# Kernel optimization log

Measured on AMD Instinct MI355X. Metric: run time of the kernel, lower is better.

## Reference

```python
import jax, jax.numpy as jnp
import numpy as np

LN_EPS = 1e-12  # default nn.LayerNorm eps used by the HF ViT config


def setup_inputs() -> dict:
    key = jax.random.key(0)
    ks = jax.random.split(key, 6)
    B, H, S, D = 2, 12, 197, 768
    Hd = D // H
    hidden_states = jax.random.normal(ks[0], (B, S, D), jnp.float32)
    # attention probs: softmax-normalized over last axis for realism
    logits = jax.random.normal(ks[1], (B, H, S, S), jnp.float32)
    attention_probs = jax.nn.softmax(logits, axis=-1)
    value_layer = jax.random.normal(ks[2], (B, H, S, Hd), jnp.float32)
    dense_weight = jax.random.normal(ks[3], (D, D), jnp.float32) * 0.02
    ln_weight = jax.random.uniform(ks[4], (D,), jnp.float32, 0.5, 1.5)
    pre_ln_states = jax.random.normal(ks[5], (B, S, D), jnp.float32)
    return {
        'hidden_states': hidden_states,
        'attention_probs': attention_probs,
        'value_layer': value_layer,
        'dense_weight': dense_weight,
        'ln_weight': ln_weight,
        'pre_ln_states': pre_ln_states,
    }


def _norm(x):
    return jnp.linalg.norm(x, axis=-1)


def _diag_bsd(x):
    # torch.diagonal(x, dim1=1, dim2=2).permute(0,2,1): (b,k,s,d)->(b,s,d)
    return jnp.transpose(jnp.diagonal(x, axis1=1, axis2=2), (0, 2, 1))


def reference(hidden_states, attention_probs, value_layer, dense_weight, ln_weight, pre_ln_states):
    B, S, D = hidden_states.shape
    H = attention_probs.shape[1]
    Hd = D // H
    # dense.weight.view(all_head, H, Hd)
    dw = dense_weight.reshape(D, H, Hd)
    transformed = jnp.einsum('bhsv,dhv->bhsd', value_layer, dw)          # (B,H,S,D)
    weighted = jnp.einsum('bhks,bhsd->bhksd', attention_probs, transformed)  # (B,H,S,S,D)
    weighted_norm = _norm(weighted)                                       # (B,H,S,S)
    summed = weighted.sum(axis=1)                                         # (B,S,S,D)
    summed_norm = _norm(summed)
    residual = jnp.einsum('sk,bsd->bskd', jnp.eye(S, dtype=hidden_states.dtype), hidden_states)
    residual_weighted = summed + residual                                 # (B,S,S,D)
    residual_weighted_norm = _norm(residual_weighted)
    # LayerNorm decomposition: variance from pre_ln_states, mean per-component
    mean = pre_ln_states.mean(-1, keepdims=True)                          # (B,S,1)
    var = ((pre_ln_states - mean) ** 2).mean(-1, keepdims=True)[:, :, None]  # (B,S,1,1)
    each_mean = residual_weighted.mean(-1, keepdims=True)
    normalized = (residual_weighted - each_mean) / jnp.sqrt(var + LN_EPS)
    post_ln = normalized * ln_weight                                      # (B,S,S,D)
    post_ln_norm = _norm(post_ln)
    # mixing ratios
    def mixing_ratio(x):
        preserving = _diag_bsd(x)
        mixing = x.sum(axis=2) - preserving
        pn, mn = _norm(preserving), _norm(mixing)
        return mn / (mn + pn)
    attn_mix = mixing_ratio(summed)
    attnres_mix = mixing_ratio(residual_weighted)
    attnresln_mix = mixing_ratio(post_ln)
    return (weighted_norm, summed_norm, residual_weighted_norm, post_ln_norm,
            post_ln, attn_mix, attnres_mix, attnresln_mix)
```

## Files before the change

kernel.cpp:

```cpp
#include <hip/hip_runtime.h>
#include <cstdint>

#define S_ 197
#define D_ 768
#define H_ 12
#define B_ 2
#define SS_ (S_*S_)

#define O_WN   0
#define O_SN   931416
#define O_RWN  1009034
#define O_PLNN 1086652
#define O_PLN  1164270
#define O_AM   60774894
#define O_ARM  60775288
#define O_ARLM 60775682

#define WS_WT   0
#define WS_T2   589824
#define WS_TN   4220928
#define WS_ACC  4225656
#define WS_SMU  4830840
#define WS_DIAG 4831628
#define WS_MUI  5134220

#define I_T 4
#define NIT 50
#define NC 2
#define JC 99

__device__ __forceinline__ float wred64(float v) {
#pragma unroll
  for (int off = 32; off > 0; off >>= 1) v += __shfl_xor(v, off);
  return v;
}

__device__ __forceinline__ void load12(const float* __restrict__ p, float t[12]) {
  const float4* q = (const float4*)p;
  float4 a = q[0], b = q[1], c = q[2];
  t[0]=a.x; t[1]=a.y; t[2]=a.z; t[3]=a.w;
  t[4]=b.x; t[5]=b.y; t[6]=b.z; t[7]=b.w;
  t[8]=c.x; t[9]=c.y; t[10]=c.z; t[11]=c.w;
}

__global__ __launch_bounds__(256) void kTranspose(const float* __restrict__ in,
                                                  float* __restrict__ outp) {
  __shared__ float tile[32][33];
  int x = blockIdx.x*32 + threadIdx.x;
  int y = blockIdx.y*32 + threadIdx.y;
#pragma unroll
  for (int k = 0; k < 32; k += 8) tile[threadIdx.y+k][threadIdx.x] = in[(y+k)*D_ + x];
  __syncthreads();
  x = blockIdx.y*32 + threadIdx.x;
  y = blockIdx.x*32 + threadIdx.y;
#pragma unroll
  for (int k = 0; k < 32; k += 8) outp[(y+k)*D_ + x] = tile[threadIdx.x][threadIdx.y+k];
}

#define TST 8
__global__ __launch_bounds__(256) void kTransform(const float* __restrict__ V,
                                                  const float* __restrict__ Wt,
                                                  float* __restrict__ T2,
                                                  float* __restrict__ tnorm) {
  int blk = blockIdx.x;
  int xcd = blk & 7; int slot = blk >> 3;
  int bh = xcd*3 + (slot % 3);
  int st = slot / 3;
  int h = bh % H_; int b = bh / H_;
  int s0 = st*TST; int ns = min(TST, S_ - s0);
  __shared__ float vt[TST*64];
  __shared__ float red[4][TST];
  int t = threadIdx.x;
  const float* Vbase = V + ((size_t)bh*S_ + s0)*64;
  for (int e = t; e < ns*64; e += 256) vt[e] = Vbase[e];
  __syncthreads();
  float acc2[TST];
#pragma unroll
  for (int s = 0; s < TST; s++) acc2[s] = 0.f;
  for (int g = 0; g < 3; g++) {
    int d = t + g*256;
    float acc[TST];
#pragma unroll
    for (int s = 0; s < TST; s++) acc[s] = 0.f;
    const float* wp = Wt + (size_t)h*64*D_ + d;
#pragma unroll 8
    for (int v = 0; v < 64; v++) {
      float wv = wp[(size_t)v*D_];
#pragma unroll
      for (int s = 0; s < TST; s++) acc[s] = fmaf(vt[s*64+v], wv, acc[s]);
    }
    for (int s = 0; s < ns; s++) {
      T2[((size_t)(b*S_ + s0+s)*H_ + h)*D_ + d] = acc[s];
      acc2[s] = fmaf(acc[s], acc[s], acc2[s]);
    }
  }
  int lane = t & 63, wq = t >> 6;
#pragma unroll
  for (int s = 0; s < TST; s++) {
    float v = wred64(acc2[s]);
    if (lane == 0) red[wq][s] = v;
  }
  __syncthreads();
  if (t < ns) {
    float v = red[0][t] + red[1][t] + red[2][t] + red[3][t];
    tnorm[bh*S_ + s0 + t] = sqrtf(v);
  }
}

__global__ __launch_bounds__(256) void kWeightedNorm(const float* __restrict__ attn,
                                                     const float* __restrict__ tnorm,
                                                     float* __restrict__ outp) {
  int idx = blockIdx.x*256 + threadIdx.x;
  if (idx < B_*H_*SS_) {
    int bh = idx / SS_;
    int s = idx % S_;
    outp[O_WN + idx] = fabsf(attn[idx]) * tnorm[bh*S_ + s];
  }
}

__global__ __launch_bounds__(768) void kMain(const float* __restrict__ attn,
                                             const float* __restrict__ hs,
                                             const float* __restrict__ lnw,
                                             const float* __restrict__ preln,
                                             const float* __restrict__ T2,
                                             float* __restrict__ outp,
                                             float* __restrict__ wsAccS,
                                             float* __restrict__ wsSmu,
                                             float* __restrict__ wsDiagS,
                                             float* __restrict__ wsMui) {
  int blk = blockIdx.x;
  int xcd = blk & 7; int slot = blk >> 3;
  int b = (xcd >> 2) & 1;
  int c = (xcd >> 1) & 1;
  int it = slot*2 + (xcd & 1);
  int i0 = it * I_T;
  int jc0 = c * JC;
  int jcE = min(jc0 + JC, S_);
  int jcW = jcE - jc0;
  int ni = min(I_T, S_ - i0);
  int tid = threadIdx.x;
  int lane = tid & 63, wv = tid >> 6;
  int dbase = lane * 12;

  __shared__ float ash[H_*I_T*JC];
  __shared__ float sAcc[I_T*D_];
  __shared__ float sSmu[12*I_T];

  int tot = H_*I_T*jcW;
  for (int e = tid; e < tot; e += 768) {
    int hh = e / (I_T*jcW); int rem = e - hh*(I_T*jcW);
    int ii = rem / jcW; int jj = rem - ii*jcW;
    int iG = i0 + ii;
    float v = 0.f;
    if (iG < S_) v = attn[((size_t)(b*H_ + hh)*S_ + iG)*S_ + (jc0 + jj)];
    ash[(hh*I_T + ii)*JC + jj] = v;
  }

  float w_[12];
  load12(lnw + dbase, w_);
  float w2s_l = 0.f;
#pragma unroll
  for (int m = 0; m < 12; m++) w2s_l = fmaf(w_[m], w_[m], w2s_l);
  float w2sum = wred64(w2s_l);

  float istd[I_T];
#pragma unroll
  for (int ii = 0; ii < I_T; ii++) {
    int iG = i0 + ii;
    istd[ii] = 0.f;
    if (iG < S_) {
      float x[12];
      load12(preln + (size_t)(b*S_ + iG)*D_ + dbase, x);
      float sx = 0.f, sx2 = 0.f;
#pragma unroll
      for (int m = 0; m < 12; m++) { sx += x[m]; sx2 = fmaf(x[m], x[m], sx2); }
      sx = wred64(sx); sx2 = wred64(sx2);
      float mu = sx * (1.0f/768.0f);
      float var = sx2 * (1.0f/768.0f) - mu*mu;
      istd[ii] = 1.0f / sqrtf(var + 1e-12f);
    }
  }

  float accS[I_T][12];
#pragma unroll
  for (int ii = 0; ii < I_T; ii++)
#pragma unroll
    for (int m = 0; m < 12; m++) accS[ii][m] = 0.f;
  float smu[I_T] = {0.f, 0.f, 0.f, 0.f};

  __syncthreads();

  for (int j = jc0 + wv; j < jcE; j += 12) {
    int jj = j - jc0;
    const float* tb = T2 + (size_t)(b*S_ + j)*H_*D_ + dbase;
    float s[I_T][12];
#pragma unroll
    for (int ii = 0; ii < I_T; ii++)
#pragma unroll
      for (int m = 0; m < 12; m++) s[ii][m] = 0.f;
#pragma unroll 2
    for (int h = 0; h < H_; h++) {
      float t[12];
      load12(tb + h*D_, t);
#pragma unroll
      for (int ii = 0; ii < I_T; ii++) {
        float ah = ash[(h*I_T + ii)*JC + jj];
#pragma unroll
        for (int m = 0; m < 12; m++) s[ii][m] = fmaf(ah, t[m], s[ii][m]);
      }
    }
#pragma unroll
    for (int ii = 0; ii < I_T; ii++) {
      int iG = i0 + ii;
      if (iG < S_) {
        bool isDiag = (j == iG);
        float rw[12];
        if (isDiag) {
          float hh[12];
          load12(hs + (size_t)(b*S_ + iG)*D_ + dbase, hh);
#pragma unroll
          for (int m = 0; m < 12; m++) rw[m] = s[ii][m] + hh[m];
        } else {
#pragma unroll
          for (int m = 0; m < 12; m++) rw[m] = s[ii][m];
        }
        float ls2 = 0.f, lrw = 0.f, lrw2 = 0.f, lrww2 = 0.f, lrw2w2 = 0.f;
#pragma unroll
        for (int m = 0; m < 12; m++) {
          ls2 = fmaf(s[ii][m], s[ii][m], ls2);
          lrw += rw[m];
          float t1 = rw[m] * w_[m];
          lrww2 = fmaf(t1, w_[m], lrww2);
          lrw2 = fmaf(rw[m], rw[m], lrw2);
          lrw2w2 = fmaf(t1, t1, lrw2w2);
        }
        ls2 = wred64(ls2); lrw = wred64(lrw); lrw2 = wred64(lrw2);
        lrww2 = wred64(lrww2); lrw2w2 = wred64(lrw2w2);
        float mu = lrw * (1.0f/768.0f);
        float q = fmaf(mu*mu, w2sum, fmaf(-2.0f*mu, lrww2, lrw2w2));
        float plnn = istd[ii] * sqrtf(fmaxf(q, 0.f));
        int oIdx = (b*S_ + iG)*S_ + j;
        if (lane == 0) {
          outp[O_SN + oIdx] = sqrtf(ls2);
          outp[O_RWN + oIdx] = sqrtf(lrw2);
          outp[O_PLNN + oIdx] = plnn;
        }
        float* po = outp + O_PLN + (size_t)oIdx*D_ + dbase;
        float a = istd[ii];
        float p[12];
#pragma unroll
        for (int m = 0; m < 12; m++) p[m] = (rw[m] - mu) * a * w_[m];
        *(float2*)po        = make_float2(p[0], p[1]);
        *(float4*)(po + 2)  = make_float4(p[2], p[3], p[4], p[5]);
        *(float4*)(po + 6)  = make_float4(p[6], p[7], p[8], p[9]);
        *(float2*)(po + 10) = make_float2(p[10], p[11]);
#pragma unroll
        for (int m = 0; m < 12; m++) accS[ii][m] += s[ii][m];
        smu[ii] += mu;
        if (isDiag) {
          float4* dp = (float4*)(wsDiagS + (size_t)(b*S_ + iG)*D_ + dbase);
          dp[0] = make_float4(s[ii][0], s[ii][1], s[ii][2],  s[ii][3]);
          dp[1] = make_float4(s[ii][4], s[ii][5], s[ii][6],  s[ii][7]);
          dp[2] = make_float4(s[ii][8], s[ii][9], s[ii][10], s[ii][11]);
          if (lane == 0) wsMui[b*S_ + iG] = mu;
        }
      }
    }
  }

  if (lane == 0) {
#pragma unroll
    for (int ii = 0; ii < I_T; ii++) sSmu[wv*I_T + ii] = smu[ii];
  }
  for (int rr = 0; rr < 12; rr++) {
    __syncthreads();
    if (wv == rr) {
#pragma unroll
      for (int ii = 0; ii < I_T; ii++) {
        if (ii < ni) {
#pragma unroll
          for (int m = 0; m < 12; m++) {
            int a = ii*D_ + dbase + m;
            sAcc[a] = (rr == 0) ? accS[ii][m] : (sAcc[a] + accS[ii][m]);
          }
        }
      }
    }
  }
  __syncthreads();
  if (tid < ni*192) {
    int ii = tid / 192; int d4 = (tid % 192) * 4;
    float4 v = *(float4*)&sAcc[ii*D_ + d4];
    *(float4*)(wsAccS + (size_t)((b*S_ + i0 + ii)*NC + c)*D_ + d4) = v;
  }
  if (tid < ni) {
    float ss = 0.f;
#pragma unroll
    for (int wq = 0; wq < 12; wq++) ss += sSmu[wq*I_T + tid];
    wsSmu[(b*S_ + i0 + tid)*NC + c] = ss;
  }
}

__global__ __launch_bounds__(256) void kMixing(const float* __restrict__ wsAccS,
                                               const float* __restrict__ wsSmu,
                                               const float* __restrict__ wsDiagS,
                                               const float* __restrict__ wsMui,
                                               const float* __restrict__ hs,
                                               const float* __restrict__ lnw,
                                               float* __restrict__ outp) {
  int bi = blockIdx.x;
  int t = threadIdx.x;
  float Smu = wsSmu[bi*2] + wsSmu[bi*2 + 1];
  float mui = wsMui[bi];
  float dmu = Smu - mui;
  float mS = 0.f, pS = 0.f, pRW = 0.f, mP = 0.f, pP = 0.f;
#pragma unroll
  for (int g = 0; g < 3; g++) {
    int d = t + g*256;
    float acc = wsAccS[(size_t)(bi*2)*D_ + d] + wsAccS[(size_t)(bi*2 + 1)*D_ + d];
    float dg = wsDiagS[(size_t)bi*D_ + d];
    float h = hs[(size_t)bi*D_ + d];
    float w = lnw[d];
    float mix = acc - dg;
    mS = fmaf(mix, mix, mS);
    pS = fmaf(dg, dg, pS);
    float drw = dg + h;
    pRW = fmaf(drw, drw, pRW);
    float mp = w * (mix - dmu);
    mP = fmaf(mp, mp, mP);
    float dp = w * (drw - mui);
    pP = fmaf(dp, dp, pP);
  }
  __shared__ float red[4][5];
  int lane = t & 63, wv = t >> 6;
  mS = wred64(mS); pS = wred64(pS); pRW = wred64(pRW); mP = wred64(mP); pP = wred64(pP);
  if (lane == 0) { red[wv][0]=mS; red[wv][1]=pS; red[wv][2]=pRW; red[wv][3]=mP; red[wv][4]=pP; }
  __syncthreads();
  if (t == 0) {
    float a0=0,a1=0,a2=0,a3=0,a4=0;
#pragma unroll
    for (int k = 0; k < 4; k++) { a0+=red[k][0]; a1+=red[k][1]; a2+=red[k][2]; a3+=red[k][3]; a4+=red[k][4]; }
    float mn = sqrtf(a0), pn = sqrtf(a1);
    outp[O_AM + bi] = mn / (mn + pn);
    float pnrw = sqrtf(a2);
    outp[O_ARM + bi] = mn / (mn + pnrw);
    float mnp = sqrtf(a3), pnp = sqrtf(a4);
    outp[O_ARLM + bi] = mnp / (mnp + pnp);
  }
}

extern "C" void kernel_launch(void* const* d_in, const int* in_sizes, int n_in,
                              void* d_out, int out_size, void* d_ws, size_t ws_size,
                              hipStream_t stream) {
  const float* hs    = (const float*)d_in[0];
  const float* attn  = (const float*)d_in[1];
  const float* V     = (const float*)d_in[2];
  const float* W     = (const float*)d_in[3];
  const float* lnw   = (const float*)d_in[4];
  const float* preln = (const float*)d_in[5];
  float* out = (float*)d_out;
  float* ws  = (float*)d_ws;

  kTranspose<<<dim3(24,24), dim3(32,8), 0, stream>>>(W, ws + WS_WT);
  kTransform<<<dim3(600), dim3(256), 0, stream>>>(V, ws + WS_WT, ws + WS_T2, ws + WS_TN);
  kWeightedNorm<<<dim3((B_*H_*SS_ + 255)/256), dim3(256), 0, stream>>>(attn, ws + WS_TN, out);
  kMain<<<dim3(B_*NIT*NC), dim3(768), 0, stream>>>(attn, hs, lnw, preln, ws + WS_T2, out,
                                                   ws + WS_ACC, ws + WS_SMU, ws + WS_DIAG, ws + WS_MUI);
  kMixing<<<dim3(B_*S_), dim3(256), 0, stream>>>(ws + WS_ACC, ws + WS_SMU, ws + WS_DIAG, ws + WS_MUI,
                                                 hs, lnw, out);
}
```

Baseline: 351.1 us.

## Fuse weighted-norm into main kernel, split columns four ways, reuse diagonal reductions

Removes the separate weighted-norm kernel by having the main kernel write |attn|*tnorm from its shared-memory attention tile, with per-head transform norms staged in shared memory. The column dimension is now split into four chunks across 400 blocks of 512 threads, replacing two chunks across 200 blocks of 768 threads. The diagonal term is left out of the accumulated sums, and its already-reduced norms are stored as three scalars, so the mixing kernel no longer reads the diagonal vectors or hidden states. The main trade-off is more partial-sum traffic in the mixing kernel, which now reads four accumulator rows per position instead of two.

```diff
diff --git a/kernel.cpp b/kernel.cpp
--- a/kernel.cpp
+++ b/kernel.cpp
@@ -16,18 +16,17 @@
 #define O_ARM  60775288
 #define O_ARLM 60775682
 
-#define WS_WT   0
-#define WS_T2   589824
-#define WS_TN   4220928
-#define WS_ACC  4225656
-#define WS_SMU  4830840
-#define WS_DIAG 4831628
-#define WS_MUI  5134220
+#define WS_T2   0
+#define WS_TN   3631104
+#define WS_ACC  3635832
+#define WS_WT   3635832
+#define WS_SMU  4846200
+#define WS_MUI  4847776
+#define WS_P3   4848170
 
 #define I_T 4
-#define NIT 50
-#define NC 2
-#define JC 99
+#define NC 4
+#define JCM 50
 
 __device__ __forceinline__ float wred64(float v) {
 #pragma unroll
@@ -107,53 +106,46 @@
   }
 }
 
-__global__ __launch_bounds__(256) void kWeightedNorm(const float* __restrict__ attn,
-                                                     const float* __restrict__ tnorm,
-                                                     float* __restrict__ outp) {
-  int idx = blockIdx.x*256 + threadIdx.x;
-  if (idx < B_*H_*SS_) {
-    int bh = idx / SS_;
-    int s = idx % S_;
-    outp[O_WN + idx] = fabsf(attn[idx]) * tnorm[bh*S_ + s];
-  }
-}
-
-__global__ __launch_bounds__(768) void kMain(const float* __restrict__ attn,
+__global__ __launch_bounds__(512) void kMain(const float* __restrict__ attn,
                                              const float* __restrict__ hs,
                                              const float* __restrict__ lnw,
                                              const float* __restrict__ preln,
                                              const float* __restrict__ T2,
+                                             const float* __restrict__ tnorm,
                                              float* __restrict__ outp,
                                              float* __restrict__ wsAccS,
                                              float* __restrict__ wsSmu,
-                                             float* __restrict__ wsDiagS,
-                                             float* __restrict__ wsMui) {
+                                             float* __restrict__ wsMui,
+                                             float* __restrict__ wsP) {
   int blk = blockIdx.x;
-  int xcd = blk & 7; int slot = blk >> 3;
-  int b = (xcd >> 2) & 1;
-  int c = (xcd >> 1) & 1;
-  int it = slot*2 + (xcd & 1);
+  int xcd = blk & 7; int it = blk >> 3;
+  int b = xcd >> 2;  int c = xcd & 3;
   int i0 = it * I_T;
-  int jc0 = c * JC;
-  int jcE = min(jc0 + JC, S_);
+  int jc0 = (c == 3) ? 149 : c*50;
+  int jcE = (c == 0) ? 50 : (c == 1) ? 100 : (c == 2) ? 149 : 197;
   int jcW = jcE - jc0;
   int ni = min(I_T, S_ - i0);
   int tid = threadIdx.x;
   int lane = tid & 63, wv = tid >> 6;
   int dbase = lane * 12;
 
-  __shared__ float ash[H_*I_T*JC];
+  __shared__ float ash[H_*I_T*JCM];
+  __shared__ float tnl[H_*JCM];
   __shared__ float sAcc[I_T*D_];
-  __shared__ float sSmu[12*I_T];
+  __shared__ float sSmu[8*I_T];
 
   int tot = H_*I_T*jcW;
-  for (int e = tid; e < tot; e += 768) {
+  for (int e = tid; e < tot; e += 512) {
     int hh = e / (I_T*jcW); int rem = e - hh*(I_T*jcW);
     int ii = rem / jcW; int jj = rem - ii*jcW;
     int iG = i0 + ii;
     float v = 0.f;
     if (iG < S_) v = attn[((size_t)(b*H_ + hh)*S_ + iG)*S_ + (jc0 + jj)];
-    ash[(hh*I_T + ii)*JC + jj] = v;
+    ash[(hh*I_T + ii)*JCM + jj] = v;
+  }
+  for (int e = tid; e < H_*jcW; e += 512) {
+    int hh = e / jcW; int jj = e - hh*jcW;
+    tnl[hh*JCM + jj] = tnorm[(b*H_ + hh)*S_ + jc0 + jj];
   }
 
   float w_[12];
@@ -190,7 +182,7 @@
 
   __syncthreads();
 
-  for (int j = jc0 + wv; j < jcE; j += 12) {
+  for (int j = jc0 + wv; j < jcE; j += 8) {
     int jj = j - jc0;
     const float* tb = T2 + (size_t)(b*S_ + j)*H_*D_ + dbase;
     float s[I_T][12];
@@ -204,7 +196,7 @@
       load12(tb + h*D_, t);
 #pragma unroll
       for (int ii = 0; ii < I_T; ii++) {
-        float ah = ash[(h*I_T + ii)*JC + jj];
+        float ah = ash[(h*I_T + ii)*JCM + jj];
 #pragma unroll
         for (int m = 0; m < 12; m++) s[ii][m] = fmaf(ah, t[m], s[ii][m]);
       }
@@ -238,7 +230,8 @@
         lrww2 = wred64(lrww2); lrw2w2 = wred64(lrw2w2);
         float mu = lrw * (1.0f/768.0f);
         float q = fmaf(mu*mu, w2sum, fmaf(-2.0f*mu, lrww2, lrw2w2));
-        float plnn = istd[ii] * sqrtf(fmaxf(q, 0.f));
+        q = fmaxf(q, 0.f);
+        float plnn = istd[ii] * sqrtf(q);
         int oIdx = (b*S_ + iG)*S_ + j;
         if (lane == 0) {
           outp[O_SN + oIdx] = sqrtf(ls2);
@@ -254,15 +247,17 @@
         *(float4*)(po + 2)  = make_float4(p[2], p[3], p[4], p[5]);
         *(float4*)(po + 6)  = make_float4(p[6], p[7], p[8], p[9]);
         *(float2*)(po + 10) = make_float2(p[10], p[11]);
-#pragma unroll
-        for (int m = 0; m < 12; m++) accS[ii][m] += s[ii][m];
         smu[ii] += mu;
         if (isDiag) {
-          float4* dp = (float4*)(wsDiagS + (size_t)(b*S_ + iG)*D_ + dbase);
-          dp[0] = make_float4(s[ii][0], s[ii][1], s[ii][2],  s[ii][3]);
-          dp[1] = make_float4(s[ii][4], s[ii][5], s[ii][6],  s[ii][7]);
-          dp[2] = make_float4(s[ii][8], s[ii][9], s[ii][10], s[ii][11]);
-          if (lane == 0) wsMui[b*S_ + iG] = mu;
+          if (lane == 0) {
+            wsMui[b*S_ + iG] = mu;
+            wsP[(b*S_ + iG)*3 + 0] = ls2;
+            wsP[(b*S_ + iG)*3 + 1] = lrw2;
+            wsP[(b*S_ + iG)*3 + 2] = q;
+          }
+        } else {
+#pragma unroll
+          for (int m = 0; m < 12; m++) accS[ii][m] += s[ii][m];
         }
       }
     }
@@ -272,7 +267,7 @@
 #pragma unroll
     for (int ii = 0; ii < I_T; ii++) sSmu[wv*I_T + ii] = smu[ii];
   }
-  for (int rr = 0; rr < 12; rr++) {
+  for (int rr = 0; rr < 8; rr++) {
     __syncthreads();
     if (wv == rr) {
 #pragma unroll
@@ -288,63 +283,64 @@
     }
   }
   __syncthreads();
-  if (tid < ni*192) {
-    int ii = tid / 192; int d4 = (tid % 192) * 4;
+  for (int e = tid; e < ni*192; e += 512) {
+    int ii = e / 192; int d4 = (e % 192) * 4;
     float4 v = *(float4*)&sAcc[ii*D_ + d4];
     *(float4*)(wsAccS + (size_t)((b*S_ + i0 + ii)*NC + c)*D_ + d4) = v;
   }
   if (tid < ni) {
     float ss = 0.f;
 #pragma unroll
-    for (int wq = 0; wq < 12; wq++) ss += sSmu[wq*I_T + tid];
+    for (int wq = 0; wq < 8; wq++) ss += sSmu[wq*I_T + tid];
     wsSmu[(b*S_ + i0 + tid)*NC + c] = ss;
+  }
+  int totW = H_*ni*jcW;
+  for (int e = tid; e < totW; e += 512) {
+    int hh = e / (ni*jcW); int rem = e - hh*(ni*jcW);
+    int ii = rem / jcW; int jj = rem - ii*jcW;
+    int iG = i0 + ii;
+    outp[O_WN + ((size_t)(b*H_ + hh)*S_ + iG)*S_ + jc0 + jj] =
+        fabsf(ash[(hh*I_T + ii)*JCM + jj]) * tnl[hh*JCM + jj];
   }
 }
 
 __global__ __launch_bounds__(256) void kMixing(const float* __restrict__ wsAccS,
                                                const float* __restrict__ wsSmu,
-                                               const float* __restrict__ wsDiagS,
                                                const float* __restrict__ wsMui,
-                                               const float* __restrict__ hs,
+                                               const float* __restrict__ wsP,
                                                const float* __restrict__ lnw,
                                                float* __restrict__ outp) {
   int bi = blockIdx.x;
   int t = threadIdx.x;
-  float Smu = wsSmu[bi*2] + wsSmu[bi*2 + 1];
+  float Smu = wsSmu[bi*4] + wsSmu[bi*4+1] + wsSmu[bi*4+2] + wsSmu[bi*4+3];
   float mui = wsMui[bi];
   float dmu = Smu - mui;
-  float mS = 0.f, pS = 0.f, pRW = 0.f, mP = 0.f, pP = 0.f;
+  float mS = 0.f, mP = 0.f;
 #pragma unroll
   for (int g = 0; g < 3; g++) {
     int d = t + g*256;
-    float acc = wsAccS[(size_t)(bi*2)*D_ + d] + wsAccS[(size_t)(bi*2 + 1)*D_ + d];
-    float dg = wsDiagS[(size_t)bi*D_ + d];
-    float h = hs[(size_t)bi*D_ + d];
+    float mix = wsAccS[((size_t)bi*4 + 0)*D_ + d] + wsAccS[((size_t)bi*4 + 1)*D_ + d]
+              + wsAccS[((size_t)bi*4 + 2)*D_ + d] + wsAccS[((size_t)bi*4 + 3)*D_ + d];
     float w = lnw[d];
-    float mix = acc - dg;
     mS = fmaf(mix, mix, mS);
-    pS = fmaf(dg, dg, pS);
-    float drw = dg + h;
-    pRW = fmaf(drw, drw, pRW);
     float mp = w * (mix - dmu);
     mP = fmaf(mp, mp, mP);
-    float dp = w * (drw - mui);
-    pP = fmaf(dp, dp, pP);
-  }
-  __shared__ float red[4][5];
+  }
+  __shared__ float red[4][2];
   int lane = t & 63, wv = t >> 6;
-  mS = wred64(mS); pS = wred64(pS); pRW = wred64(pRW); mP = wred64(mP); pP = wred64(pP);
-  if (lane == 0) { red[wv][0]=mS; red[wv][1]=pS; red[wv][2]=pRW; red[wv][3]=mP; red[wv][4]=pP; }
+  mS = wred64(mS); mP = wred64(mP);
+  if (lane == 0) { red[wv][0] = mS; red[wv][1] = mP; }
   __syncthreads();
   if (t == 0) {
-    float a0=0,a1=0,a2=0,a3=0,a4=0;
-#pragma unroll
-    for (int k = 0; k < 4; k++) { a0+=red[k][0]; a1+=red[k][1]; a2+=red[k][2]; a3+=red[k][3]; a4+=red[k][4]; }
-    float mn = sqrtf(a0), pn = sqrtf(a1);
-    outp[O_AM + bi] = mn / (mn + pn);
-    float pnrw = sqrtf(a2);
-    outp[O_ARM + bi] = mn / (mn + pnrw);
-    float mnp = sqrtf(a3), pnp = sqrtf(a4);
+    float a0 = 0.f, a1 = 0.f;
+#pragma unroll
+    for (int k = 0; k < 4; k++) { a0 += red[k][0]; a1 += red[k][1]; }
+    float mn = sqrtf(a0), mnp = sqrtf(a1);
+    float pn   = sqrtf(wsP[bi*3 + 0]);
+    float pnrw = sqrtf(wsP[bi*3 + 1]);
+    float pnp  = sqrtf(wsP[bi*3 + 2]);
+    outp[O_AM   + bi] = mn / (mn + pn);
+    outp[O_ARM  + bi] = mn / (mn + pnrw);
     outp[O_ARLM + bi] = mnp / (mnp + pnp);
   }
 }
@@ -363,9 +359,8 @@
 
   kTranspose<<<dim3(24,24), dim3(32,8), 0, stream>>>(W, ws + WS_WT);
   kTransform<<<dim3(600), dim3(256), 0, stream>>>(V, ws + WS_WT, ws + WS_T2, ws + WS_TN);
-  kWeightedNorm<<<dim3((B_*H_*SS_ + 255)/256), dim3(256), 0, stream>>>(attn, ws + WS_TN, out);
-  kMain<<<dim3(B_*NIT*NC), dim3(768), 0, stream>>>(attn, hs, lnw, preln, ws + WS_T2, out,
-                                                   ws + WS_ACC, ws + WS_SMU, ws + WS_DIAG, ws + WS_MUI);
-  kMixing<<<dim3(B_*S_), dim3(256), 0, stream>>>(ws + WS_ACC, ws + WS_SMU, ws + WS_DIAG, ws + WS_MUI,
-                                                 hs, lnw, out);
-}
+  kMain<<<dim3(400), dim3(512), 0, stream>>>(attn, hs, lnw, preln, ws + WS_T2, ws + WS_TN,
+                                             out, ws + WS_ACC, ws + WS_SMU, ws + WS_MUI, ws + WS_P3);
+  kMixing<<<dim3(B_*S_), dim3(256), 0, stream>>>(ws + WS_ACC, ws + WS_SMU, ws + WS_MUI, ws + WS_P3,
+                                                 lnw, out);
+}
```

Result: slower. 370.4 us (+5.5%).
